# Performance work log

Hardware: AMD Instinct MI355X
Metric: run time of the kernel (lower is better)

Reference implementation:

```python
import jax, jax.numpy as jnp
import numpy as np

B, T, D = 8, 2048, 128


def setup_inputs() -> dict:
    key = jax.random.key(0)
    kq, kk, kv = jax.random.split(key, 3)
    q = jax.random.normal(kq, (B, T, D), dtype=jnp.float32)
    k = jax.random.normal(kk, (B, T, D), dtype=jnp.float32)
    v = jax.random.normal(kv, (B, T, D), dtype=jnp.float32)
    # causal mask, broadcast over batch; 0 -> masked
    mask = jnp.tril(jnp.ones((T, T), dtype=jnp.int32))[None, :, :]
    mode = jnp.float32(0.5)  # learnable scalar parameter (init 0.5)
    return {"q": q, "k": k, "v": v, "mask": mask, "mode": mode}


def reference(q, k, v, mask, mode):
    scale = D ** (-0.5)
    # meson score: -(Q K^T) * scale
    meson = -jnp.einsum("btd,bsd->bts", q, k) * scale
    # baryon score: Q against K with feature dim rolled by 1
    k_perm = jnp.roll(k, shift=1, axis=-1)
    baryon = jnp.einsum("btd,bsd->bts", q, k_perm) * scale
    alpha = jax.nn.sigmoid(mode)
    attn = alpha * meson + (1.0 - alpha) * baryon
    attn = jnp.where(mask == 0, -jnp.inf, attn)
    attn = jax.nn.softmax(attn, axis=-1)
    return jnp.einsum("bts,bsd->btd", attn, v)
```

## Files before the change

kernel.cpp:

```cpp
#include <hip/hip_runtime.h>
#include <hip/hip_bf16.h>
#include <cstdint>
#include <cstddef>


typedef __attribute__((ext_vector_type(8))) short short8;
typedef __attribute__((ext_vector_type(4))) float f32x4;

#define T_DIM 2048
#define D_DIM 128
#define B_DIM 8
#define MAXSEG 4

__device__ __forceinline__ unsigned short f2bf(float f) {
  unsigned u = __builtin_bit_cast(unsigned, f);
  u += 0x7FFFu + ((u >> 16) & 1u);
  return (unsigned short)(u >> 16);
}
__device__ __forceinline__ float bf2f(unsigned short u) {
  return __uint_as_float(((unsigned)u) << 16);
}
__device__ __forceinline__ void gload_lds16(const void* g, void* l) {
  __builtin_amdgcn_global_load_lds(
      (const __attribute__((address_space(1))) unsigned int*)g,
      (__attribute__((address_space(3))) unsigned int*)l, 16, 0, 0);
}

__global__ __launch_bounds__(256) void prep_all(
    const float* __restrict__ q, const float* __restrict__ k, const float* __restrict__ v,
    const float* __restrict__ modep,
    unsigned short* __restrict__ qbf, unsigned short* __restrict__ kbf,
    unsigned short* __restrict__ vt)
{
  __shared__ unsigned short tile[64 * 136];
  const int b = blockIdx.x, s0 = blockIdx.y * 64;
  const int tid = threadIdx.x;
  const float alpha = 1.f / (1.f + __expf(-modep[0]));
  const float scale = 0.08838834764831845f;
  const float ca = -alpha * scale, cb = (1.f - alpha) * scale;

#pragma unroll
  for (int u = 0; u < 4; ++u) {
    int c = u * 256 + tid;
    int r = c >> 4, c8 = c & 15;
    size_t row = (size_t)b * T_DIM + s0 + r;
    float4 ka = *(const float4*)(k + row * D_DIM + c8 * 8);
    float4 kb2 = *(const float4*)(k + row * D_DIM + c8 * 8 + 4);
    short8 ko = { (short)f2bf(ka.x), (short)f2bf(ka.y), (short)f2bf(ka.z), (short)f2bf(ka.w),
                  (short)f2bf(kb2.x), (short)f2bf(kb2.y), (short)f2bf(kb2.z), (short)f2bf(kb2.w) };
    *(short8*)(kbf + row * D_DIM + c8 * 8) = ko;
    const float* qr = q + row * D_DIM;
    float e[9];
    float4 f0 = *(const float4*)(qr + c8 * 8);
    float4 f1 = *(const float4*)(qr + c8 * 8 + 4);
    e[0] = f0.x; e[1] = f0.y; e[2] = f0.z; e[3] = f0.w;
    e[4] = f1.x; e[5] = f1.y; e[6] = f1.z; e[7] = f1.w;
    e[8] = qr[(c8 * 8 + 8) & 127];
    short8 qo;
#pragma unroll
    for (int j = 0; j < 8; ++j) qo[j] = (short)f2bf(ca * e[j] + cb * e[j + 1]);
    *(short8*)(qbf + row * D_DIM + c8 * 8) = qo;
    float4 va = *(const float4*)(v + row * D_DIM + c8 * 8);
    float4 vb2 = *(const float4*)(v + row * D_DIM + c8 * 8 + 4);
    short8 vo = { (short)f2bf(va.x), (short)f2bf(va.y), (short)f2bf(va.z), (short)f2bf(va.w),
                  (short)f2bf(vb2.x), (short)f2bf(vb2.y), (short)f2bf(vb2.z), (short)f2bf(vb2.w) };
    *(short8*)(tile + r * 136 + c8 * 8) = vo;
  }
  __syncthreads();
#pragma unroll
  for (int u = 0; u < 8; ++u) {
    int c = u * 256 + tid;
    int d = c >> 4, sq = c & 15;
    ushort4 o = { tile[(sq * 4 + 0) * 136 + d], tile[(sq * 4 + 1) * 136 + d],
                  tile[(sq * 4 + 2) * 136 + d], tile[(sq * 4 + 3) * 136 + d] };
    *(ushort4*)(vt + ((size_t)b * D_DIM + d) * T_DIM + s0 + sq * 4) = o;
  }
}

__global__ __launch_bounds__(128, 2) void attn_kernel(
    const unsigned short* __restrict__ qbf, const unsigned short* __restrict__ kbf,
    const unsigned short* __restrict__ vt, float* __restrict__ out,
    unsigned short* __restrict__ po, float* __restrict__ ml, int segt)
{
  __shared__ uint4 smem4[2304];
  char* smem = (char*)smem4;
  const int tid = threadIdx.x;
  const int w = tid >> 6, lane = tid & 63;
  const int t16 = lane & 15, g = lane >> 4;
  const int b = blockIdx.x;
  const int qc = blockIdx.y, seg = blockIdx.z;
  const int nt = qc + 1;
  const int nseg = (nt + segt - 1) / segt;
  if (seg >= nseg) return;
  const int t0 = seg * segt;
  const int t1 = min(nt, t0 + segt);
  const int qb = qc * 64 + w * 32;

  char* kb = smem;
  char* vb = smem + 16384;
  char* pw = smem + 32768 + w * 2048;
  const unsigned short* kbase = kbf + (size_t)b * T_DIM * D_DIM;
  const unsigned short* vbase = vt + (size_t)b * D_DIM * T_DIM;

  short8 qf[2][4];
#pragma unroll
  for (int mt = 0; mt < 2; ++mt) {
    const unsigned short* qr = qbf + ((size_t)b * T_DIM + qb + mt * 16 + t16) * D_DIM + g * 8;
#pragma unroll
    for (int dd = 0; dd < 4; ++dd) qf[mt][dd] = *(const short8*)(qr + dd * 32);
  }

  f32x4 acc[2][8];
#pragma unroll
  for (int mt = 0; mt < 2; ++mt)
#pragma unroll
    for (int dt = 0; dt < 8; ++dt) acc[mt][dt] = (f32x4){0.f, 0.f, 0.f, 0.f};
  float mrun[2][4], lrun[2][4];
#pragma unroll
  for (int mt = 0; mt < 2; ++mt)
#pragma unroll
    for (int r = 0; r < 4; ++r) { mrun[mt][r] = -1e30f; lrun[mt][r] = 0.f; }

  for (int kt = t0; kt < t1; ++kt) {
    const int kv0 = kt * 64;
    __syncthreads();
#pragma unroll
    for (int u = 0; u < 8; ++u) {
      int s_loc = w * 32 + u * 4 + (lane >> 4);
      int slot = (lane & 15) ^ (s_loc & 7);
      gload_lds16(kbase + (size_t)(kv0 + s_loc) * D_DIM + slot * 8,
                  kb + w * 8192 + u * 1024);
    }
#pragma unroll
    for (int u = 0; u < 8; ++u) {
      int d_loc = w * 64 + u * 8 + (lane >> 3);
      int vslot = (lane & 7) ^ (d_loc & 7);
      gload_lds16(vbase + (size_t)d_loc * T_DIM + kv0 + vslot * 8,
                  vb + w * 8192 + u * 1024);
    }
    __syncthreads();

    f32x4 sj[2][4];
#pragma unroll
    for (int jt = 0; jt < 4; ++jt) {
      int s = jt * 16 + t16;
      int rb = s * 256, swz = (s & 7) << 4;
      f32x4 s0 = (f32x4){0.f, 0.f, 0.f, 0.f};
      f32x4 s1 = (f32x4){0.f, 0.f, 0.f, 0.f};
#pragma unroll
      for (int dd = 0; dd < 4; ++dd) {
        short8 kf = *(const short8*)(kb + ((rb + dd * 64 + g * 16) ^ swz));
        s0 = __builtin_amdgcn_mfma_f32_16x16x32_bf16(qf[0][dd], kf, s0, 0, 0, 0);
        s1 = __builtin_amdgcn_mfma_f32_16x16x32_bf16(qf[1][dd], kf, s1, 0, 0, 0);
      }
      sj[0][jt] = s0; sj[1][jt] = s1;
    }

    const bool needmask = (kt == nt - 1);
#pragma unroll
    for (int mt = 0; mt < 2; ++mt) {
      if (needmask) {
#pragma unroll
        for (int jt = 0; jt < 4; ++jt) {
          int sg = kv0 + jt * 16 + t16;
#pragma unroll
          for (int r = 0; r < 4; ++r) {
            int tg = qb + mt * 16 + 4 * g + r;
            if (sg > tg) sj[mt][jt][r] = -1e30f;
          }
        }
      }
      float tm[4];
#pragma unroll
      for (int r = 0; r < 4; ++r)
        tm[r] = fmaxf(fmaxf(sj[mt][0][r], sj[mt][1][r]), fmaxf(sj[mt][2][r], sj[mt][3][r]));
#pragma unroll
      for (int r = 0; r < 4; ++r) {
        tm[r] = fmaxf(tm[r], __shfl_xor(tm[r], 1));
        tm[r] = fmaxf(tm[r], __shfl_xor(tm[r], 2));
        tm[r] = fmaxf(tm[r], __shfl_xor(tm[r], 4));
        tm[r] = fmaxf(tm[r], __shfl_xor(tm[r], 8));
      }
      float corr[4], rs[4];
#pragma unroll
      for (int r = 0; r < 4; ++r) {
        float mnew = fmaxf(mrun[mt][r], tm[r]);
        corr[r] = __expf(mrun[mt][r] - mnew);
        mrun[mt][r] = mnew;
        rs[r] = 0.f;
      }
#pragma unroll
      for (int jt = 0; jt < 4; ++jt)
#pragma unroll
        for (int r = 0; r < 4; ++r) {
          float p = __expf(sj[mt][jt][r] - mrun[mt][r]);
          sj[mt][jt][r] = p;
          rs[r] += p;
        }
#pragma unroll
      for (int r = 0; r < 4; ++r) {
        rs[r] += __shfl_xor(rs[r], 1);
        rs[r] += __shfl_xor(rs[r], 2);
        rs[r] += __shfl_xor(rs[r], 4);
        rs[r] += __shfl_xor(rs[r], 8);
        lrun[mt][r] = lrun[mt][r] * corr[r] + rs[r];
      }
#pragma unroll
      for (int dt = 0; dt < 8; ++dt)
#pragma unroll
        for (int r = 0; r < 4; ++r) acc[mt][dt][r] *= corr[r];

#pragma unroll
      for (int jt = 0; jt < 4; ++jt)
#pragma unroll
        for (int r = 0; r < 4; ++r) {
          int rloc = 4 * g + r;
          *(unsigned short*)(pw + rloc * 128 + ((2 * (jt * 16 + t16)) ^ ((rloc & 7) << 4))) =
              f2bf(sj[mt][jt][r]);
        }

#pragma unroll
      for (int k0 = 0; k0 < 2; ++k0) {
        short8 pf = *(const short8*)(pw + t16 * 128 + ((k0 * 64 + g * 16) ^ ((t16 & 7) << 4)));
#pragma unroll
        for (int dt = 0; dt < 8; ++dt) {
          int d = dt * 16 + t16;
          short8 vf = *(const short8*)(vb + d * 128 + (((k0 * 4 + g) << 4) ^ ((d & 7) << 4)));
          acc[mt][dt] = __builtin_amdgcn_mfma_f32_16x16x32_bf16(pf, vf, acc[mt][dt], 0, 0, 0);
        }
      }
    }
  }

  if (nseg == 1) {
#pragma unroll
    for (int mt = 0; mt < 2; ++mt)
#pragma unroll
      for (int r = 0; r < 4; ++r) {
        float inv = 1.0f / lrun[mt][r];
#pragma unroll
        for (int dt = 0; dt < 8; ++dt)
          out[((size_t)b * T_DIM + qb + mt * 16 + 4 * g + r) * D_DIM + dt * 16 + t16] =
              acc[mt][dt][r] * inv;
      }
  } else {
    const int slot = (b * 32 + qc) * MAXSEG + seg;
    unsigned short* pob = po + (size_t)slot * 8192;
#pragma unroll
    for (int mt = 0; mt < 2; ++mt)
#pragma unroll
      for (int r = 0; r < 4; ++r) {
        int rb = w * 32 + mt * 16 + 4 * g + r;
#pragma unroll
        for (int dt = 0; dt < 8; ++dt)
          pob[rb * 128 + dt * 16 + t16] = f2bf(acc[mt][dt][r]);
      }
    if (t16 == 0) {
#pragma unroll
      for (int mt = 0; mt < 2; ++mt)
#pragma unroll
        for (int r = 0; r < 4; ++r) {
          int rb = w * 32 + mt * 16 + 4 * g + r;
          ml[(size_t)slot * 128 + rb] = mrun[mt][r];
          ml[(size_t)slot * 128 + 64 + rb] = lrun[mt][r];
        }
    }
  }
}

__global__ __launch_bounds__(256) void combine_kernel(
    const unsigned short* __restrict__ po, const float* __restrict__ ml,
    float* __restrict__ out, int segt)
{
  const int tid = threadIdx.x;
  const int b = blockIdx.x;
  const int qc = segt + (int)blockIdx.y;
  const int nt = qc + 1;
  const int nseg = (nt + segt - 1) / segt;
  const int slot0 = (b * 32 + qc) * MAXSEG;

  __shared__ float wgt[64][MAXSEG];
  if (tid < 64) {
    float M = -1e30f;
    for (int s = 0; s < nseg; ++s)
      M = fmaxf(M, ml[(size_t)(slot0 + s) * 128 + tid]);
    float L = 0.f;
    for (int s = 0; s < nseg; ++s) {
      float e = __expf(ml[(size_t)(slot0 + s) * 128 + tid] - M);
      wgt[tid][s] = e;
      L += e * ml[(size_t)(slot0 + s) * 128 + 64 + tid];
    }
    float invL = 1.f / L;
    for (int s = 0; s < nseg; ++s) wgt[tid][s] *= invL;
  }
  __syncthreads();

#pragma unroll
  for (int it = 0; it < 4; ++it) {
    int vid = it * 256 + tid;
    int r = vid >> 4, ch = vid & 15;
    float o[8] = {0.f, 0.f, 0.f, 0.f, 0.f, 0.f, 0.f, 0.f};
    for (int s = 0; s < nseg; ++s) {
      short8 pv = *(const short8*)(po + (size_t)(slot0 + s) * 8192 + r * 128 + ch * 8);
      float ws = wgt[r][s];
#pragma unroll
      for (int j = 0; j < 8; ++j) o[j] += ws * bf2f((unsigned short)pv[j]);
    }
    float* dst = out + ((size_t)b * T_DIM + qc * 64 + r) * D_DIM + ch * 8;
    *(float4*)(dst) = (float4){o[0], o[1], o[2], o[3]};
    *(float4*)(dst + 4) = (float4){o[4], o[5], o[6], o[7]};
  }
}

extern "C" void kernel_launch(void* const* d_in, const int* in_sizes, int n_in,
                              void* d_out, int out_size, void* d_ws, size_t ws_size,
                              hipStream_t stream) {
  const float* q = (const float*)d_in[0];
  const float* k = (const float*)d_in[1];
  const float* v = (const float*)d_in[2];
  const float* mode = (const float*)d_in[4];
  float* out = (float*)d_out;

  char* ws = (char*)d_ws;
  unsigned short* qbf = (unsigned short*)(ws);
  unsigned short* kbf = (unsigned short*)(ws + 4194304);
  unsigned short* vtb = (unsigned short*)(ws + 8388608);
  unsigned short* po  = (unsigned short*)(ws + 12582912);
  float*          ml  = (float*)(ws + 29360128);

  const bool split = ws_size >= 29884416ULL;
  const int segt = split ? 8 : 32;

  prep_all<<<dim3(B_DIM, T_DIM / 64), 256, 0, stream>>>(q, k, v, mode, qbf, kbf, vtb);
  attn_kernel<<<dim3(B_DIM, 32, split ? MAXSEG : 1), 128, 0, stream>>>(
      qbf, kbf, vtb, out, po, ml, segt);
  if (split)
    combine_kernel<<<dim3(B_DIM, 24), 256, 0, stream>>>(po, ml, out, segt);
}
```

Baseline: 58.60 us.

## Split KV range per wave with 32-row query chunks and direct global K/V reads

```diff
diff --git a/kernel.cpp b/kernel.cpp
--- a/kernel.cpp
+++ b/kernel.cpp
@@ -10,7 +10,8 @@
 #define T_DIM 2048
 #define D_DIM 128
 #define B_DIM 8
-#define MAXSEG 4
+#define POSLOTS_PER_B 346
+#define MLSLOTS_PER_B 410
 
 __device__ __forceinline__ unsigned short f2bf(float f) {
   unsigned u = __builtin_bit_cast(unsigned, f);
@@ -20,25 +21,14 @@
 __device__ __forceinline__ float bf2f(unsigned short u) {
   return __uint_as_float(((unsigned)u) << 16);
 }
-__device__ __forceinline__ void gload_lds16(const void* g, void* l) {
-  __builtin_amdgcn_global_load_lds(
-      (const __attribute__((address_space(1))) unsigned int*)g,
-      (__attribute__((address_space(3))) unsigned int*)l, 16, 0, 0);
-}
-
-__global__ __launch_bounds__(256) void prep_all(
-    const float* __restrict__ q, const float* __restrict__ k, const float* __restrict__ v,
-    const float* __restrict__ modep,
-    unsigned short* __restrict__ qbf, unsigned short* __restrict__ kbf,
-    unsigned short* __restrict__ vt)
+
+__global__ __launch_bounds__(256) void prep_kv(
+    const float* __restrict__ k, const float* __restrict__ v,
+    unsigned short* __restrict__ kbf, unsigned short* __restrict__ vt)
 {
   __shared__ unsigned short tile[64 * 136];
   const int b = blockIdx.x, s0 = blockIdx.y * 64;
   const int tid = threadIdx.x;
-  const float alpha = 1.f / (1.f + __expf(-modep[0]));
-  const float scale = 0.08838834764831845f;
-  const float ca = -alpha * scale, cb = (1.f - alpha) * scale;
-
 #pragma unroll
   for (int u = 0; u < 4; ++u) {
     int c = u * 256 + tid;
@@ -49,17 +39,6 @@
     short8 ko = { (short)f2bf(ka.x), (short)f2bf(ka.y), (short)f2bf(ka.z), (short)f2bf(ka.w),
                   (short)f2bf(kb2.x), (short)f2bf(kb2.y), (short)f2bf(kb2.z), (short)f2bf(kb2.w) };
     *(short8*)(kbf + row * D_DIM + c8 * 8) = ko;
-    const float* qr = q + row * D_DIM;
-    float e[9];
-    float4 f0 = *(const float4*)(qr + c8 * 8);
-    float4 f1 = *(const float4*)(qr + c8 * 8 + 4);
-    e[0] = f0.x; e[1] = f0.y; e[2] = f0.z; e[3] = f0.w;
-    e[4] = f1.x; e[5] = f1.y; e[6] = f1.z; e[7] = f1.w;
-    e[8] = qr[(c8 * 8 + 8) & 127];
-    short8 qo;
-#pragma unroll
-    for (int j = 0; j < 8; ++j) qo[j] = (short)f2bf(ca * e[j] + cb * e[j + 1]);
-    *(short8*)(qbf + row * D_DIM + c8 * 8) = qo;
     float4 va = *(const float4*)(v + row * D_DIM + c8 * 8);
     float4 vb2 = *(const float4*)(v + row * D_DIM + c8 * 8 + 4);
     short8 vo = { (short)f2bf(va.x), (short)f2bf(va.y), (short)f2bf(va.z), (short)f2bf(va.w),
@@ -77,37 +56,51 @@
   }
 }
 
-__global__ __launch_bounds__(128, 2) void attn_kernel(
-    const unsigned short* __restrict__ qbf, const unsigned short* __restrict__ kbf,
-    const unsigned short* __restrict__ vt, float* __restrict__ out,
-    unsigned short* __restrict__ po, float* __restrict__ ml, int segt)
+__global__ __launch_bounds__(256, 4) void attn_kernel(
+    const float* __restrict__ q, const unsigned short* __restrict__ kbf,
+    const unsigned short* __restrict__ vt, const float* __restrict__ modep,
+    float* __restrict__ out, unsigned short* __restrict__ po, float* __restrict__ ml)
 {
-  __shared__ uint4 smem4[2304];
-  char* smem = (char*)smem4;
+  __shared__ char psm[4 * 2048];
   const int tid = threadIdx.x;
   const int w = tid >> 6, lane = tid & 63;
   const int t16 = lane & 15, g = lane >> 4;
   const int b = blockIdx.x;
-  const int qc = blockIdx.y, seg = blockIdx.z;
-  const int nt = qc + 1;
-  const int nseg = (nt + segt - 1) / segt;
-  if (seg >= nseg) return;
-  const int t0 = seg * segt;
-  const int t1 = min(nt, t0 + segt);
-  const int qb = qc * 64 + w * 32;
-
-  char* kb = smem;
-  char* vb = smem + 16384;
-  char* pw = smem + 32768 + w * 2048;
+  const int c = blockIdx.y;
+  const int s = blockIdx.z * 4 + w;
+  const int nt = (c + 2) >> 1;
+  const int tps = (nt + 7) >> 3;
+  const int t0 = s * tps;
+  if (t0 >= nt) return;
+  const int t1 = min(nt, t0 + tps);
+  const int nsl = (nt + tps - 1) / tps;
+  const int qb = c * 32;
+
+  char* pw = psm + w * 2048;
   const unsigned short* kbase = kbf + (size_t)b * T_DIM * D_DIM;
   const unsigned short* vbase = vt + (size_t)b * D_DIM * T_DIM;
 
+  const float alpha = 1.f / (1.f + __expf(-modep[0]));
+  const float scale = 0.08838834764831845f;
+  const float ca = -alpha * scale, cb = (1.f - alpha) * scale;
   short8 qf[2][4];
 #pragma unroll
   for (int mt = 0; mt < 2; ++mt) {
-    const unsigned short* qr = qbf + ((size_t)b * T_DIM + qb + mt * 16 + t16) * D_DIM + g * 8;
-#pragma unroll
-    for (int dd = 0; dd < 4; ++dd) qf[mt][dd] = *(const short8*)(qr + dd * 32);
+    const float* qr = q + ((size_t)b * T_DIM + qb + mt * 16 + t16) * D_DIM;
+#pragma unroll
+    for (int dd = 0; dd < 4; ++dd) {
+      int dstart = dd * 32 + g * 8;
+      float e[9];
+      float4 f0 = *(const float4*)(qr + dstart);
+      float4 f1 = *(const float4*)(qr + dstart + 4);
+      e[0] = f0.x; e[1] = f0.y; e[2] = f0.z; e[3] = f0.w;
+      e[4] = f1.x; e[5] = f1.y; e[6] = f1.z; e[7] = f1.w;
+      e[8] = qr[(dstart + 8) & 127];
+      short8 qv;
+#pragma unroll
+      for (int i = 0; i < 8; ++i) qv[i] = (short)f2bf(ca * e[i] + cb * e[i + 1]);
+      qf[mt][dd] = qv;
+    }
   }
 
   f32x4 acc[2][8];
@@ -123,33 +116,16 @@
 
   for (int kt = t0; kt < t1; ++kt) {
     const int kv0 = kt * 64;
-    __syncthreads();
-#pragma unroll
-    for (int u = 0; u < 8; ++u) {
-      int s_loc = w * 32 + u * 4 + (lane >> 4);
-      int slot = (lane & 15) ^ (s_loc & 7);
-      gload_lds16(kbase + (size_t)(kv0 + s_loc) * D_DIM + slot * 8,
-                  kb + w * 8192 + u * 1024);
-    }
-#pragma unroll
-    for (int u = 0; u < 8; ++u) {
-      int d_loc = w * 64 + u * 8 + (lane >> 3);
-      int vslot = (lane & 7) ^ (d_loc & 7);
-      gload_lds16(vbase + (size_t)d_loc * T_DIM + kv0 + vslot * 8,
-                  vb + w * 8192 + u * 1024);
-    }
-    __syncthreads();
 
     f32x4 sj[2][4];
 #pragma unroll
     for (int jt = 0; jt < 4; ++jt) {
-      int s = jt * 16 + t16;
-      int rb = s * 256, swz = (s & 7) << 4;
+      const unsigned short* kr = kbase + (size_t)(kv0 + jt * 16 + t16) * D_DIM + g * 8;
       f32x4 s0 = (f32x4){0.f, 0.f, 0.f, 0.f};
       f32x4 s1 = (f32x4){0.f, 0.f, 0.f, 0.f};
 #pragma unroll
       for (int dd = 0; dd < 4; ++dd) {
-        short8 kf = *(const short8*)(kb + ((rb + dd * 64 + g * 16) ^ swz));
+        short8 kf = *(const short8*)(kr + dd * 32);
         s0 = __builtin_amdgcn_mfma_f32_16x16x32_bf16(qf[0][dd], kf, s0, 0, 0, 0);
         s1 = __builtin_amdgcn_mfma_f32_16x16x32_bf16(qf[1][dd], kf, s1, 0, 0, 0);
       }
@@ -224,15 +200,15 @@
         short8 pf = *(const short8*)(pw + t16 * 128 + ((k0 * 64 + g * 16) ^ ((t16 & 7) << 4)));
 #pragma unroll
         for (int dt = 0; dt < 8; ++dt) {
-          int d = dt * 16 + t16;
-          short8 vf = *(const short8*)(vb + d * 128 + (((k0 * 4 + g) << 4) ^ ((d & 7) << 4)));
+          const unsigned short* vr = vbase + (size_t)(dt * 16 + t16) * T_DIM + kv0 + k0 * 32 + g * 8;
+          short8 vf = *(const short8*)vr;
           acc[mt][dt] = __builtin_amdgcn_mfma_f32_16x16x32_bf16(pf, vf, acc[mt][dt], 0, 0, 0);
         }
       }
     }
   }
 
-  if (nseg == 1) {
+  if (nsl == 1) {
 #pragma unroll
     for (int mt = 0; mt < 2; ++mt)
 #pragma unroll
@@ -244,25 +220,41 @@
               acc[mt][dt][r] * inv;
       }
   } else {
-    const int slot = (b * 32 + qc) * MAXSEG + seg;
-    unsigned short* pob = po + (size_t)slot * 8192;
-#pragma unroll
-    for (int mt = 0; mt < 2; ++mt)
-#pragma unroll
-      for (int r = 0; r < 4; ++r) {
-        int rb = w * 32 + mt * 16 + 4 * g + r;
-#pragma unroll
-        for (int dt = 0; dt < 8; ++dt)
-          pob[rb * 128 + dt * 16 + t16] = f2bf(acc[mt][dt][r]);
-      }
+    int pofs = 0;
+    for (int cc = 0; cc < c; ++cc) {
+      int ntc = (cc + 2) >> 1, tpsc = (ntc + 7) >> 3;
+      pofs += (ntc + tpsc - 1) / tpsc - 1;
+    }
+    if (s == 0) {
+#pragma unroll
+      for (int mt = 0; mt < 2; ++mt)
+#pragma unroll
+        for (int r = 0; r < 4; ++r)
+#pragma unroll
+          for (int dt = 0; dt < 8; ++dt)
+            out[((size_t)b * T_DIM + qb + mt * 16 + 4 * g + r) * D_DIM + dt * 16 + t16] =
+                acc[mt][dt][r];
+    } else {
+      unsigned short* pob = po + ((size_t)b * POSLOTS_PER_B + pofs + (s - 1)) * 4096;
+#pragma unroll
+      for (int mt = 0; mt < 2; ++mt)
+#pragma unroll
+        for (int r = 0; r < 4; ++r) {
+          int rb = mt * 16 + 4 * g + r;
+#pragma unroll
+          for (int dt = 0; dt < 8; ++dt)
+            pob[rb * 128 + dt * 16 + t16] = f2bf(acc[mt][dt][r]);
+        }
+    }
     if (t16 == 0) {
+      const size_t mlslot = (size_t)b * MLSLOTS_PER_B + pofs + c + s;
 #pragma unroll
       for (int mt = 0; mt < 2; ++mt)
 #pragma unroll
         for (int r = 0; r < 4; ++r) {
-          int rb = w * 32 + mt * 16 + 4 * g + r;
-          ml[(size_t)slot * 128 + rb] = mrun[mt][r];
-          ml[(size_t)slot * 128 + 64 + rb] = lrun[mt][r];
+          int rb = mt * 16 + 4 * g + r;
+          ml[mlslot * 64 + rb] = mrun[mt][r];
+          ml[mlslot * 64 + 32 + rb] = lrun[mt][r];
         }
     }
   }
@@ -270,45 +262,56 @@
 
 __global__ __launch_bounds__(256) void combine_kernel(
     const unsigned short* __restrict__ po, const float* __restrict__ ml,
-    float* __restrict__ out, int segt)
+    float* __restrict__ out)
 {
   const int tid = threadIdx.x;
   const int b = blockIdx.x;
-  const int qc = segt + (int)blockIdx.y;
-  const int nt = qc + 1;
-  const int nseg = (nt + segt - 1) / segt;
-  const int slot0 = (b * 32 + qc) * MAXSEG;
-
-  __shared__ float wgt[64][MAXSEG];
-  if (tid < 64) {
+  const int c = 2 + (int)blockIdx.y;
+  const int nt = (c + 2) >> 1;
+  const int tps = (nt + 7) >> 3;
+  const int nsl = (nt + tps - 1) / tps;
+  int pofs = 0;
+  for (int cc = 0; cc < c; ++cc) {
+    int ntc = (cc + 2) >> 1, tpsc = (ntc + 7) >> 3;
+    pofs += (ntc + tpsc - 1) / tpsc - 1;
+  }
+  const size_t mlbase = (size_t)b * MLSLOTS_PER_B + pofs + c;
+  const size_t pobase = (size_t)b * POSLOTS_PER_B + pofs;
+
+  __shared__ float wgt[32][8];
+  if (tid < 32) {
     float M = -1e30f;
-    for (int s = 0; s < nseg; ++s)
-      M = fmaxf(M, ml[(size_t)(slot0 + s) * 128 + tid]);
+    for (int s = 0; s < nsl; ++s)
+      M = fmaxf(M, ml[(mlbase + s) * 64 + tid]);
     float L = 0.f;
-    for (int s = 0; s < nseg; ++s) {
-      float e = __expf(ml[(size_t)(slot0 + s) * 128 + tid] - M);
+    for (int s = 0; s < nsl; ++s) {
+      float e = __expf(ml[(mlbase + s) * 64 + tid] - M);
       wgt[tid][s] = e;
-      L += e * ml[(size_t)(slot0 + s) * 128 + 64 + tid];
+      L += e * ml[(mlbase + s) * 64 + 32 + tid];
     }
     float invL = 1.f / L;
-    for (int s = 0; s < nseg; ++s) wgt[tid][s] *= invL;
+    for (int s = 0; s < nsl; ++s) wgt[tid][s] *= invL;
   }
   __syncthreads();
 
 #pragma unroll
-  for (int it = 0; it < 4; ++it) {
+  for (int it = 0; it < 2; ++it) {
     int vid = it * 256 + tid;
     int r = vid >> 4, ch = vid & 15;
-    float o[8] = {0.f, 0.f, 0.f, 0.f, 0.f, 0.f, 0.f, 0.f};
-    for (int s = 0; s < nseg; ++s) {
-      short8 pv = *(const short8*)(po + (size_t)(slot0 + s) * 8192 + r * 128 + ch * 8);
+    float* op = out + ((size_t)b * T_DIM + c * 32 + r) * D_DIM + ch * 8;
+    float4 a0 = *(const float4*)op;
+    float4 a1 = *(const float4*)(op + 4);
+    float w0 = wgt[r][0];
+    float o[8] = { w0 * a0.x, w0 * a0.y, w0 * a0.z, w0 * a0.w,
+                   w0 * a1.x, w0 * a1.y, w0 * a1.z, w0 * a1.w };
+    for (int s = 1; s < nsl; ++s) {
+      short8 pv = *(const short8*)(po + (pobase + s - 1) * 4096 + r * 128 + ch * 8);
       float ws = wgt[r][s];
 #pragma unroll
       for (int j = 0; j < 8; ++j) o[j] += ws * bf2f((unsigned short)pv[j]);
     }
-    float* dst = out + ((size_t)b * T_DIM + qc * 64 + r) * D_DIM + ch * 8;
-    *(float4*)(dst) = (float4){o[0], o[1], o[2], o[3]};
-    *(float4*)(dst + 4) = (float4){o[4], o[5], o[6], o[7]};
+    *(float4*)op = (float4){o[0], o[1], o[2], o[3]};
+    *(float4*)(op + 4) = (float4){o[4], o[5], o[6], o[7]};
   }
 }
 
@@ -322,18 +325,12 @@
   float* out = (float*)d_out;
 
   char* ws = (char*)d_ws;
-  unsigned short* qbf = (unsigned short*)(ws);
-  unsigned short* kbf = (unsigned short*)(ws + 4194304);
-  unsigned short* vtb = (unsigned short*)(ws + 8388608);
-  unsigned short* po  = (unsigned short*)(ws + 12582912);
-  float*          ml  = (float*)(ws + 29360128);
-
-  const bool split = ws_size >= 29884416ULL;
-  const int segt = split ? 8 : 32;
-
-  prep_all<<<dim3(B_DIM, T_DIM / 64), 256, 0, stream>>>(q, k, v, mode, qbf, kbf, vtb);
-  attn_kernel<<<dim3(B_DIM, 32, split ? MAXSEG : 1), 128, 0, stream>>>(
-      qbf, kbf, vtb, out, po, ml, segt);
-  if (split)
-    combine_kernel<<<dim3(B_DIM, 24), 256, 0, stream>>>(po, ml, out, segt);
-}
+  unsigned short* kbf = (unsigned short*)(ws);
+  unsigned short* vtb = (unsigned short*)(ws + 4194304);
+  unsigned short* po  = (unsigned short*)(ws + 8388608);
+  float*          ml  = (float*)(ws + 31064064);
+
+  prep_kv<<<dim3(B_DIM, T_DIM / 64), 256, 0, stream>>>(k, v, kbf, vtb);
+  attn_kernel<<<dim3(B_DIM, 64, 2), 256, 0, stream>>>(q, kbf, vtb, mode, out, po, ml);
+  combine_kernel<<<dim3(B_DIM, 62), 256, 0, stream>>>(po, ml, out);
+}
```

New measurement: 194.2 us. +231.4%, slower.

## Double-buffer K/V tiles, widen to 128-query blocks, add lazy rescale split-K

Applied to the files above, without the earlier changes.

```diff
diff --git a/kernel.cpp b/kernel.cpp
--- a/kernel.cpp
+++ b/kernel.cpp
@@ -10,7 +10,9 @@
 #define T_DIM 2048
 #define D_DIM 128
 #define B_DIM 8
-#define MAXSEG 4
+#define SEGT 4
+#define POSLOTS_PER_B 56
+#define MLSLOTS_PER_B 72
 
 __device__ __forceinline__ unsigned short f2bf(float f) {
   unsigned u = __builtin_bit_cast(unsigned, f);
@@ -77,28 +79,27 @@
   }
 }
 
-__global__ __launch_bounds__(128, 2) void attn_kernel(
+__global__ __launch_bounds__(256, 2) void attn_kernel(
     const unsigned short* __restrict__ qbf, const unsigned short* __restrict__ kbf,
     const unsigned short* __restrict__ vt, float* __restrict__ out,
-    unsigned short* __restrict__ po, float* __restrict__ ml, int segt)
+    unsigned short* __restrict__ po, float* __restrict__ ml)
 {
-  __shared__ uint4 smem4[2304];
+  __shared__ uint4 smem4[4608];
   char* smem = (char*)smem4;
   const int tid = threadIdx.x;
   const int w = tid >> 6, lane = tid & 63;
   const int t16 = lane & 15, g = lane >> 4;
   const int b = blockIdx.x;
-  const int qc = blockIdx.y, seg = blockIdx.z;
-  const int nt = qc + 1;
-  const int nseg = (nt + segt - 1) / segt;
-  if (seg >= nseg) return;
-  const int t0 = seg * segt;
-  const int t1 = min(nt, t0 + segt);
-  const int qb = qc * 64 + w * 32;
-
-  char* kb = smem;
-  char* vb = smem + 16384;
-  char* pw = smem + 32768 + w * 2048;
+  const int c = blockIdx.y;
+  const int s = blockIdx.z;
+  const int nt = 2 * c + 2;
+  const int nseg = (c + 2) >> 1;
+  if (s >= nseg) return;
+  const int t0 = s * SEGT;
+  const int t1 = min(nt, t0 + SEGT);
+  const int qb = c * 128 + w * 32;
+
+  char* pw = smem + 65536 + w * 2048;
   const unsigned short* kbase = kbf + (size_t)b * T_DIM * D_DIM;
   const unsigned short* vbase = vt + (size_t)b * D_DIM * T_DIM;
 
@@ -115,154 +116,204 @@
   for (int mt = 0; mt < 2; ++mt)
 #pragma unroll
     for (int dt = 0; dt < 8; ++dt) acc[mt][dt] = (f32x4){0.f, 0.f, 0.f, 0.f};
-  float mrun[2][4], lrun[2][4];
+  float mrun[2][4], lsum[2][4];
 #pragma unroll
   for (int mt = 0; mt < 2; ++mt)
 #pragma unroll
-    for (int r = 0; r < 4; ++r) { mrun[mt][r] = -1e30f; lrun[mt][r] = 0.f; }
-
-  for (int kt = t0; kt < t1; ++kt) {
+    for (int r = 0; r < 4; ++r) { mrun[mt][r] = -1e30f; lsum[mt][r] = 0.f; }
+
+  auto stage = [&](int cur, int kt) {
     const int kv0 = kt * 64;
-    __syncthreads();
-#pragma unroll
-    for (int u = 0; u < 8; ++u) {
-      int s_loc = w * 32 + u * 4 + (lane >> 4);
+    char* kb = smem + cur * 16384;
+    char* vb = smem + 32768 + cur * 16384;
+#pragma unroll
+    for (int u = 0; u < 4; ++u) {
+      int s_loc = w * 16 + u * 4 + (lane >> 4);
       int slot = (lane & 15) ^ (s_loc & 7);
       gload_lds16(kbase + (size_t)(kv0 + s_loc) * D_DIM + slot * 8,
-                  kb + w * 8192 + u * 1024);
-    }
-#pragma unroll
-    for (int u = 0; u < 8; ++u) {
-      int d_loc = w * 64 + u * 8 + (lane >> 3);
+                  kb + w * 4096 + u * 1024);
+    }
+#pragma unroll
+    for (int u = 0; u < 4; ++u) {
+      int d_loc = w * 32 + u * 8 + (lane >> 3);
       int vslot = (lane & 7) ^ (d_loc & 7);
       gload_lds16(vbase + (size_t)d_loc * T_DIM + kv0 + vslot * 8,
-                  vb + w * 8192 + u * 1024);
-    }
+                  vb + w * 4096 + u * 1024);
+    }
+  };
+
+  stage(0, t0);
+  __syncthreads();
+  int cur = 0;
+
+  for (int kt = t0; kt < t1; ++kt) {
+    if (kt + 1 < t1) stage(cur ^ 1, kt + 1);
+    const int kv0 = kt * 64;
+
+    if (kv0 <= qb + 31) {
+      char* kb = smem + cur * 16384;
+      char* vb = smem + 32768 + cur * 16384;
+
+      f32x4 sj[2][4];
+#pragma unroll
+      for (int jt = 0; jt < 4; ++jt) {
+        int srow = jt * 16 + t16;
+        int rb = srow * 256, swz = (srow & 7) << 4;
+        f32x4 s0 = (f32x4){0.f, 0.f, 0.f, 0.f};
+        f32x4 s1 = (f32x4){0.f, 0.f, 0.f, 0.f};
+#pragma unroll
+        for (int dd = 0; dd < 4; ++dd) {
+          short8 kf = *(const short8*)(kb + ((rb + dd * 64 + g * 16) ^ swz));
+          s0 = __builtin_amdgcn_mfma_f32_16x16x32_bf16(qf[0][dd], kf, s0, 0, 0, 0);
+          s1 = __builtin_amdgcn_mfma_f32_16x16x32_bf16(qf[1][dd], kf, s1, 0, 0, 0);
+        }
+        sj[0][jt] = s0; sj[1][jt] = s1;
+      }
+
+      if (kv0 + 63 > qb) {
+#pragma unroll
+        for (int mt = 0; mt < 2; ++mt)
+#pragma unroll
+          for (int jt = 0; jt < 4; ++jt) {
+            int sg = kv0 + jt * 16 + t16;
+#pragma unroll
+            for (int r = 0; r < 4; ++r) {
+              int tg = qb + mt * 16 + 4 * g + r;
+              if (sg > tg) sj[mt][jt][r] = -1e30f;
+            }
+          }
+      }
+
+      float lm[2][4];
+      int ok = 1;
+#pragma unroll
+      for (int mt = 0; mt < 2; ++mt)
+#pragma unroll
+        for (int r = 0; r < 4; ++r) {
+          lm[mt][r] = fmaxf(fmaxf(sj[mt][0][r], sj[mt][1][r]),
+                            fmaxf(sj[mt][2][r], sj[mt][3][r]));
+          ok &= (lm[mt][r] <= mrun[mt][r] + 8.0f);
+        }
+      if (!__all(ok)) {
+#pragma unroll
+        for (int mt = 0; mt < 2; ++mt) {
+          float tm[4];
+#pragma unroll
+          for (int r = 0; r < 4; ++r) tm[r] = lm[mt][r];
+#pragma unroll
+          for (int r = 0; r < 4; ++r) {
+            tm[r] = fmaxf(tm[r], __shfl_xor(tm[r], 1));
+            tm[r] = fmaxf(tm[r], __shfl_xor(tm[r], 2));
+            tm[r] = fmaxf(tm[r], __shfl_xor(tm[r], 4));
+            tm[r] = fmaxf(tm[r], __shfl_xor(tm[r], 8));
+          }
+#pragma unroll
+          for (int r = 0; r < 4; ++r) {
+            float mnew = fmaxf(mrun[mt][r], tm[r]);
+            float corr = __expf(mrun[mt][r] - mnew);
+            mrun[mt][r] = mnew;
+            lsum[mt][r] *= corr;
+#pragma unroll
+            for (int dt = 0; dt < 8; ++dt) acc[mt][dt][r] *= corr;
+          }
+        }
+      }
+
+#pragma unroll
+      for (int mt = 0; mt < 2; ++mt) {
+        float ls[4] = {0.f, 0.f, 0.f, 0.f};
+#pragma unroll
+        for (int jt = 0; jt < 4; ++jt)
+#pragma unroll
+          for (int r = 0; r < 4; ++r) {
+            float p = __expf(sj[mt][jt][r] - mrun[mt][r]);
+            sj[mt][jt][r] = p;
+            ls[r] += p;
+          }
+#pragma unroll
+        for (int r = 0; r < 4; ++r) lsum[mt][r] += ls[r];
+#pragma unroll
+        for (int jt = 0; jt < 4; ++jt)
+#pragma unroll
+          for (int r = 0; r < 4; ++r) {
+            int rloc = 4 * g + r;
+            *(unsigned short*)(pw + rloc * 128 + ((2 * (jt * 16 + t16)) ^ ((rloc & 7) << 4))) =
+                f2bf(sj[mt][jt][r]);
+          }
+#pragma unroll
+        for (int k0 = 0; k0 < 2; ++k0) {
+          short8 pf = *(const short8*)(pw + t16 * 128 + ((k0 * 64 + g * 16) ^ ((t16 & 7) << 4)));
+#pragma unroll
+          for (int dt = 0; dt < 8; ++dt) {
+            int d = dt * 16 + t16;
+            short8 vf = *(const short8*)(vb + d * 128 + (((k0 * 4 + g) << 4) ^ ((d & 7) << 4)));
+            acc[mt][dt] = __builtin_amdgcn_mfma_f32_16x16x32_bf16(pf, vf, acc[mt][dt], 0, 0, 0);
+          }
+        }
+      }
+    }
+
     __syncthreads();
-
-    f32x4 sj[2][4];
-#pragma unroll
-    for (int jt = 0; jt < 4; ++jt) {
-      int s = jt * 16 + t16;
-      int rb = s * 256, swz = (s & 7) << 4;
-      f32x4 s0 = (f32x4){0.f, 0.f, 0.f, 0.f};
-      f32x4 s1 = (f32x4){0.f, 0.f, 0.f, 0.f};
-#pragma unroll
-      for (int dd = 0; dd < 4; ++dd) {
-        short8 kf = *(const short8*)(kb + ((rb + dd * 64 + g * 16) ^ swz));
-        s0 = __builtin_amdgcn_mfma_f32_16x16x32_bf16(qf[0][dd], kf, s0, 0, 0, 0);
-        s1 = __builtin_amdgcn_mfma_f32_16x16x32_bf16(qf[1][dd], kf, s1, 0, 0, 0);
-      }
-      sj[0][jt] = s0; sj[1][jt] = s1;
-    }
-
-    const bool needmask = (kt == nt - 1);
-#pragma unroll
-    for (int mt = 0; mt < 2; ++mt) {
-      if (needmask) {
-#pragma unroll
-        for (int jt = 0; jt < 4; ++jt) {
-          int sg = kv0 + jt * 16 + t16;
-#pragma unroll
-          for (int r = 0; r < 4; ++r) {
-            int tg = qb + mt * 16 + 4 * g + r;
-            if (sg > tg) sj[mt][jt][r] = -1e30f;
-          }
-        }
-      }
-      float tm[4];
-#pragma unroll
-      for (int r = 0; r < 4; ++r)
-        tm[r] = fmaxf(fmaxf(sj[mt][0][r], sj[mt][1][r]), fmaxf(sj[mt][2][r], sj[mt][3][r]));
+    cur ^= 1;
+  }
+
+  float lred[2][4];
+#pragma unroll
+  for (int mt = 0; mt < 2; ++mt)
+#pragma unroll
+    for (int r = 0; r < 4; ++r) {
+      float v0 = lsum[mt][r];
+      v0 += __shfl_xor(v0, 1);
+      v0 += __shfl_xor(v0, 2);
+      v0 += __shfl_xor(v0, 4);
+      v0 += __shfl_xor(v0, 8);
+      lred[mt][r] = v0;
+    }
+
+  if (nseg == 1) {
+#pragma unroll
+    for (int mt = 0; mt < 2; ++mt)
 #pragma unroll
       for (int r = 0; r < 4; ++r) {
-        tm[r] = fmaxf(tm[r], __shfl_xor(tm[r], 1));
-        tm[r] = fmaxf(tm[r], __shfl_xor(tm[r], 2));
-        tm[r] = fmaxf(tm[r], __shfl_xor(tm[r], 4));
-        tm[r] = fmaxf(tm[r], __shfl_xor(tm[r], 8));
-      }
-      float corr[4], rs[4];
-#pragma unroll
-      for (int r = 0; r < 4; ++r) {
-        float mnew = fmaxf(mrun[mt][r], tm[r]);
-        corr[r] = __expf(mrun[mt][r] - mnew);
-        mrun[mt][r] = mnew;
-        rs[r] = 0.f;
-      }
-#pragma unroll
-      for (int jt = 0; jt < 4; ++jt)
-#pragma unroll
-        for (int r = 0; r < 4; ++r) {
-          float p = __expf(sj[mt][jt][r] - mrun[mt][r]);
-          sj[mt][jt][r] = p;
-          rs[r] += p;
-        }
-#pragma unroll
-      for (int r = 0; r < 4; ++r) {
-        rs[r] += __shfl_xor(rs[r], 1);
-        rs[r] += __shfl_xor(rs[r], 2);
-        rs[r] += __shfl_xor(rs[r], 4);
-        rs[r] += __shfl_xor(rs[r], 8);
-        lrun[mt][r] = lrun[mt][r] * corr[r] + rs[r];
-      }
-#pragma unroll
-      for (int dt = 0; dt < 8; ++dt)
-#pragma unroll
-        for (int r = 0; r < 4; ++r) acc[mt][dt][r] *= corr[r];
-
-#pragma unroll
-      for (int jt = 0; jt < 4; ++jt)
-#pragma unroll
-        for (int r = 0; r < 4; ++r) {
-          int rloc = 4 * g + r;
-          *(unsigned short*)(pw + rloc * 128 + ((2 * (jt * 16 + t16)) ^ ((rloc & 7) << 4))) =
-              f2bf(sj[mt][jt][r]);
-        }
-
-#pragma unroll
-      for (int k0 = 0; k0 < 2; ++k0) {
-        short8 pf = *(const short8*)(pw + t16 * 128 + ((k0 * 64 + g * 16) ^ ((t16 & 7) << 4)));
-#pragma unroll
-        for (int dt = 0; dt < 8; ++dt) {
-          int d = dt * 16 + t16;
-          short8 vf = *(const short8*)(vb + d * 128 + (((k0 * 4 + g) << 4) ^ ((d & 7) << 4)));
-          acc[mt][dt] = __builtin_amdgcn_mfma_f32_16x16x32_bf16(pf, vf, acc[mt][dt], 0, 0, 0);
-        }
-      }
-    }
-  }
-
-  if (nseg == 1) {
-#pragma unroll
-    for (int mt = 0; mt < 2; ++mt)
-#pragma unroll
-      for (int r = 0; r < 4; ++r) {
-        float inv = 1.0f / lrun[mt][r];
+        float inv = 1.0f / lred[mt][r];
 #pragma unroll
         for (int dt = 0; dt < 8; ++dt)
           out[((size_t)b * T_DIM + qb + mt * 16 + 4 * g + r) * D_DIM + dt * 16 + t16] =
               acc[mt][dt][r] * inv;
       }
   } else {
-    const int slot = (b * 32 + qc) * MAXSEG + seg;
-    unsigned short* pob = po + (size_t)slot * 8192;
-#pragma unroll
-    for (int mt = 0; mt < 2; ++mt)
-#pragma unroll
-      for (int r = 0; r < 4; ++r) {
-        int rb = w * 32 + mt * 16 + 4 * g + r;
-#pragma unroll
-        for (int dt = 0; dt < 8; ++dt)
-          pob[rb * 128 + dt * 16 + t16] = f2bf(acc[mt][dt][r]);
-      }
-    if (t16 == 0) {
+    int pofs = 0;
+    for (int cc = 0; cc < c; ++cc) pofs += ((cc + 2) >> 1) - 1;
+    if (s == 0) {
+#pragma unroll
+      for (int mt = 0; mt < 2; ++mt)
+#pragma unroll
+        for (int r = 0; r < 4; ++r)
+#pragma unroll
+          for (int dt = 0; dt < 8; ++dt)
+            out[((size_t)b * T_DIM + qb + mt * 16 + 4 * g + r) * D_DIM + dt * 16 + t16] =
+                acc[mt][dt][r];
+    } else {
+      unsigned short* pob = po + ((size_t)b * POSLOTS_PER_B + pofs + (s - 1)) * 16384;
 #pragma unroll
       for (int mt = 0; mt < 2; ++mt)
 #pragma unroll
         for (int r = 0; r < 4; ++r) {
           int rb = w * 32 + mt * 16 + 4 * g + r;
-          ml[(size_t)slot * 128 + rb] = mrun[mt][r];
-          ml[(size_t)slot * 128 + 64 + rb] = lrun[mt][r];
+#pragma unroll
+          for (int dt = 0; dt < 8; ++dt)
+            pob[rb * 128 + dt * 16 + t16] = f2bf(acc[mt][dt][r]);
+        }
+    }
+    if (t16 == 0) {
+      const size_t mlslot = (size_t)b * MLSLOTS_PER_B + pofs + c + s;
+#pragma unroll
+      for (int mt = 0; mt < 2; ++mt)
+#pragma unroll
+        for (int r = 0; r < 4; ++r) {
+          int rb = w * 32 + mt * 16 + 4 * g + r;
+          ml[mlslot * 256 + rb] = mrun[mt][r];
+          ml[mlslot * 256 + 128 + rb] = lred[mt][r];
         }
     }
   }
@@ -270,25 +321,27 @@
 
 __global__ __launch_bounds__(256) void combine_kernel(
     const unsigned short* __restrict__ po, const float* __restrict__ ml,
-    float* __restrict__ out, int segt)
+    float* __restrict__ out)
 {
   const int tid = threadIdx.x;
   const int b = blockIdx.x;
-  const int qc = segt + (int)blockIdx.y;
-  const int nt = qc + 1;
-  const int nseg = (nt + segt - 1) / segt;
-  const int slot0 = (b * 32 + qc) * MAXSEG;
-
-  __shared__ float wgt[64][MAXSEG];
-  if (tid < 64) {
+  const int c = 2 + (int)blockIdx.y;
+  const int nseg = (c + 2) >> 1;
+  int pofs = 0;
+  for (int cc = 0; cc < c; ++cc) pofs += ((cc + 2) >> 1) - 1;
+  const size_t mlbase = (size_t)b * MLSLOTS_PER_B + pofs + c;
+  const size_t pobase = (size_t)b * POSLOTS_PER_B + pofs;
+
+  __shared__ float wgt[128][8];
+  if (tid < 128) {
     float M = -1e30f;
     for (int s = 0; s < nseg; ++s)
-      M = fmaxf(M, ml[(size_t)(slot0 + s) * 128 + tid]);
+      M = fmaxf(M, ml[(mlbase + s) * 256 + tid]);
     float L = 0.f;
     for (int s = 0; s < nseg; ++s) {
-      float e = __expf(ml[(size_t)(slot0 + s) * 128 + tid] - M);
+      float e = __expf(ml[(mlbase + s) * 256 + tid] - M);
       wgt[tid][s] = e;
-      L += e * ml[(size_t)(slot0 + s) * 128 + 64 + tid];
+      L += e * ml[(mlbase + s) * 256 + 128 + tid];
     }
     float invL = 1.f / L;
     for (int s = 0; s < nseg; ++s) wgt[tid][s] *= invL;
@@ -296,19 +349,23 @@
   __syncthreads();
 
 #pragma unroll
-  for (int it = 0; it < 4; ++it) {
+  for (int it = 0; it < 8; ++it) {
     int vid = it * 256 + tid;
     int r = vid >> 4, ch = vid & 15;
-    float o[8] = {0.f, 0.f, 0.f, 0.f, 0.f, 0.f, 0.f, 0.f};
-    for (int s = 0; s < nseg; ++s) {
-      short8 pv = *(const short8*)(po + (size_t)(slot0 + s) * 8192 + r * 128 + ch * 8);
+    float* op = out + ((size_t)b * T_DIM + c * 128 + r) * D_DIM + ch * 8;
+    float4 a0 = *(const float4*)op;
+    float4 a1 = *(const float4*)(op + 4);
+    float w0 = wgt[r][0];
+    float o[8] = { w0 * a0.x, w0 * a0.y, w0 * a0.z, w0 * a0.w,
+                   w0 * a1.x, w0 * a1.y, w0 * a1.z, w0 * a1.w };
+    for (int s = 1; s < nseg; ++s) {
+      short8 pv = *(const short8*)(po + (pobase + s - 1) * 16384 + r * 128 + ch * 8);
       float ws = wgt[r][s];
 #pragma unroll
       for (int j = 0; j < 8; ++j) o[j] += ws * bf2f((unsigned short)pv[j]);
     }
-    float* dst = out + ((size_t)b * T_DIM + qc * 64 + r) * D_DIM + ch * 8;
-    *(float4*)(dst) = (float4){o[0], o[1], o[2], o[3]};
-    *(float4*)(dst + 4) = (float4){o[4], o[5], o[6], o[7]};
+    *(float4*)op = (float4){o[0], o[1], o[2], o[3]};
+    *(float4*)(op + 4) = (float4){o[4], o[5], o[6], o[7]};
   }
 }
 
@@ -326,14 +383,9 @@
   unsigned short* kbf = (unsigned short*)(ws + 4194304);
   unsigned short* vtb = (unsigned short*)(ws + 8388608);
   unsigned short* po  = (unsigned short*)(ws + 12582912);
-  float*          ml  = (float*)(ws + 29360128);
-
-  const bool split = ws_size >= 29884416ULL;
-  const int segt = split ? 8 : 32;
+  float*          ml  = (float*)(ws + 27262976);
 
   prep_all<<<dim3(B_DIM, T_DIM / 64), 256, 0, stream>>>(q, k, v, mode, qbf, kbf, vtb);
-  attn_kernel<<<dim3(B_DIM, 32, split ? MAXSEG : 1), 128, 0, stream>>>(
-      qbf, kbf, vtb, out, po, ml, segt);
-  if (split)
-    combine_kernel<<<dim3(B_DIM, 24), 256, 0, stream>>>(po, ml, out, segt);
-}
+  attn_kernel<<<dim3(B_DIM, 16, 8), 256, 0, stream>>>(qbf, kbf, vtb, out, po, ml);
+  combine_kernel<<<dim3(B_DIM, 14), 256, 0, stream>>>(po, ml, out);
+}
```

New measurement: 61.61 us. 1.05x slower.
